# Optimization experiments

Hardware: AMD Instinct MI355X
Metric: run time of the kernel (lower is better)

The kernel has to match this reference:

```python
import jax, jax.numpy as jnp
import numpy as np

EPS = 1e-7

def squash(s, axis=-1):
    # s * ||s||^2 / (1 + ||s||^2) / ||s||
    sq_norm = jnp.sum(jnp.square(s), axis=axis, keepdims=True)
    scale = sq_norm / (1.0 + sq_norm) / jnp.sqrt(sq_norm + EPS)
    return scale * s

def setup_inputs() -> dict:
    key = jax.random.key(0)
    k1, k2 = jax.random.split(key)
    B, I, K = 64, 2048, 16   # batch, input_num_capsule, input_dim_capsule
    N, D = 32, 32            # num_capsule, dim_capsule
    inputs = jax.random.normal(k1, (B, I, K), dtype=jnp.float32)
    W = jax.random.normal(k2, (N, I, D, K), dtype=jnp.float32) * 0.05
    return {"inputs": inputs, "W": W}

def reference(inputs, W, routings=3):
    # u_hat[b,n,i,d] = sum_k inputs[b,i,k] * W[n,i,d,k]
    # (tile over n + per-sample batch_dot in the original, fused here)
    u_hat = jnp.einsum('bik,nidk->bnid', inputs, W)  # [B,N,I,D]
    B, N, I, D = u_hat.shape
    b = jnp.zeros((B, N, I), dtype=u_hat.dtype)
    outputs = None
    for r in range(routings):
        c = jax.nn.softmax(b, axis=1)                          # softmax over num_capsule
        s = jnp.einsum('bni,bnid->bnd', c, u_hat)              # weighted sum over input caps
        outputs = squash(s)                                    # [B,N,D]
        if r < routings - 1:
            b = b + jnp.einsum('bnd,bnid->bni', outputs, u_hat)  # agreement update
    return outputs
```

## Files before the change

kernel.cpp:

```cpp
#include <hip/hip_runtime.h>
#include <hip/hip_bf16.h>
#include <math.h>

#define B_ 64
#define I_ 2048
#define K_ 16
#define N_ 32
#define D_ 32
#define CH_ 32
#define SCH_ 16

typedef __attribute__((ext_vector_type(8))) short short8_t;
typedef __attribute__((ext_vector_type(4))) float f32x4_t;

#define OFF_INT   0u
#define OFF_CT    2097152u
#define OFF_BT    6291456u
#define OFF_SPART 10485760u
#define OFF_OUTT  11534336u
#define OFF_XFRAG 11599872u
#define OFF_WFS   12648448u
#define OFF_WFU   29425664u

__device__ __forceinline__ unsigned int pk_bf16(float lo, float hi) {
    union { __hip_bfloat162 h2; unsigned int u; } cv;
    cv.h2 = __float22bfloat162_rn(float2{lo, hi});
    return cv.u;
}

__global__ __launch_bounds__(256) void k_transpose(const float* __restrict__ in,
                                                   float* __restrict__ inT) {
    __shared__ float lds[B_][K_ + 1];
    const int i = blockIdx.x;
    const int t = threadIdx.x;
    const int b = t >> 2, kq = t & 3;
    const float4 v = *(const float4*)(in + ((size_t)b * I_ + i) * K_ + kq * 4);
    lds[b][kq * 4 + 0] = v.x; lds[b][kq * 4 + 1] = v.y;
    lds[b][kq * 4 + 2] = v.z; lds[b][kq * 4 + 3] = v.w;
    __syncthreads();
#pragma unroll
    for (int q = 0; q < 4; ++q) {
        const int j = t + q * 256;
        const int k = j >> 6, bb = j & 63;
        inT[(size_t)i * (K_ * B_) + j] = lds[bb][k];
    }
}

__global__ __launch_bounds__(256) void k_xfrag(const float* __restrict__ in,
                                               uint4* __restrict__ xfrag) {
    const int tid = blockIdx.x * 256 + threadIdx.x;
    const int l = tid & 63, kk = (tid >> 6) & 1023, m = tid >> 16;
    const int b = m * 16 + (l & 15), g = l >> 4;
    const int i = 2 * kk + (g >> 1), k0 = 8 * (g & 1);
    const float* src = in + ((size_t)b * I_ + i) * K_ + k0;
    const float4 f0 = *(const float4*)src;
    const float4 f1 = *(const float4*)(src + 4);
    uint4 o;
    o.x = pk_bf16(f0.x, f0.y); o.y = pk_bf16(f0.z, f0.w);
    o.z = pk_bf16(f1.x, f1.y); o.w = pk_bf16(f1.z, f1.w);
    xfrag[tid] = o;
}

__global__ __launch_bounds__(256) void k_wpack(const float* __restrict__ W,
                                               uint4* __restrict__ wfs,
                                               uint4* __restrict__ wfu) {
    __shared__ __align__(16) float lds[2048];
    const int c = blockIdx.x;
    const int n = blockIdx.y;
    const int t = threadIdx.x;
    const float4* s4 = (const float4*)(W + ((size_t)n * I_ + c * 4) * 512);
    float4* d4 = (float4*)lds;
    d4[t] = s4[t];
    d4[t + 256] = s4[t + 256];
    __syncthreads();
    {
        const int il = t >> 6, l = t & 63, g = l >> 4, kl = l & 15;
        const float* base = lds + il * 512;
        union { unsigned int u[4]; uint4 q; } o;
#pragma unroll
        for (int p = 0; p < 4; ++p)
            o.u[p] = pk_bf16(base[(8 * g + 2 * p) * 16 + kl],
                             base[(8 * g + 2 * p + 1) * 16 + kl]);
        wfu[((size_t)n * I_ + c * 4 + il) * 64 + l] = o.q;
    }
    {
        const int kkl = t >> 7, r = t & 127, nt = r >> 6, l = r & 63, g = l >> 4;
        const float* p = lds + kkl * 1024 + (g >> 1) * 512 + nt * 256
                         + (l & 15) * 16 + (g & 1) * 8;
        const float4 f0 = *(const float4*)p;
        const float4 f1 = *(const float4*)(p + 4);
        union { unsigned int u[4]; uint4 q; } o;
        o.u[0] = pk_bf16(f0.x, f0.y); o.u[1] = pk_bf16(f0.z, f0.w);
        o.u[2] = pk_bf16(f1.x, f1.y); o.u[3] = pk_bf16(f1.z, f1.w);
        wfs[(((size_t)n * 1024 + c * 2 + kkl) * 2 + nt) * 64 + l] = o.q;
    }
}

template<int UNIFORM>
__global__ __launch_bounds__(512, 2) void k_sweep_mfma(const uint4* __restrict__ wfs,
                                                       const uint4* __restrict__ xfrag,
                                                       const float* __restrict__ cT,
                                                       float* __restrict__ spart) {
    __shared__ float red[2][B_][D_ + 1];
    const int n = blockIdx.y, ch = blockIdx.x;
    const int t = threadIdx.x, w = t >> 6, l = t & 63;
    const int m = w >> 1, ks = w & 1;

    f32x4_t acc0 = {0.f, 0.f, 0.f, 0.f};
    f32x4_t acc1 = {0.f, 0.f, 0.f, 0.f};

    const uint4* xf = xfrag + (size_t)m * 65536 + l;
    const uint4* wf = wfs + (size_t)n * (1024 * 128) + l;
    const int kk0 = ch * 64 + ks * 32;

    for (int tt = 0; tt < 32; ++tt) {
        const int kk = kk0 + tt;
        union { uint4 q; unsigned int u[4]; } xv;
        xv.q = xf[(size_t)kk * 64];
        union { unsigned int u[4]; short8_t v; } af;
        if (UNIFORM) {
            af.u[0] = xv.u[0]; af.u[1] = xv.u[1];
            af.u[2] = xv.u[2]; af.u[3] = xv.u[3];
        } else {
            const float c = cT[((size_t)n * I_ + 2 * kk + (l >> 5)) * B_
                               + m * 16 + (l & 15)];
#pragma unroll
            for (int p = 0; p < 4; ++p) {
                const unsigned int uu = xv.u[p];
                const float lo = __uint_as_float(uu << 16);
                const float hi = __uint_as_float(uu & 0xffff0000u);
                af.u[p] = pk_bf16(lo * c, hi * c);
            }
        }
        union { uint4 q; short8_t v; } b0, b1;
        b0.q = wf[(size_t)kk * 128];
        b1.q = wf[(size_t)kk * 128 + 64];

        acc0 = __builtin_amdgcn_mfma_f32_16x16x32_bf16(af.v, b0.v, acc0, 0, 0, 0);
        acc1 = __builtin_amdgcn_mfma_f32_16x16x32_bf16(af.v, b1.v, acc1, 0, 0, 0);
    }

#pragma unroll
    for (int r = 0; r < 4; ++r) {
        const int row = m * 16 + (l >> 4) * 4 + r;
        red[ks][row][(l & 15)]      = acc0[r];
        red[ks][row][16 + (l & 15)] = acc1[r];
    }
    __syncthreads();
#pragma unroll
    for (int q = 0; q < 4; ++q) {
        const int j = q * 512 + t;
        const int b = j >> 5, d = j & 31;
        spart[((size_t)n * SCH_ + ch) * (B_ * D_) + j] = red[0][b][d] + red[1][b][d];
    }
}

template<int FINAL>
__global__ __launch_bounds__(256) void k_reduce(const float* __restrict__ spart,
                                                float* __restrict__ outT,
                                                float* __restrict__ out,
                                                float prescale) {
    const int gt = blockIdx.x * 256 + threadIdx.x;
    const int n = gt >> 11;
    const int rem = gt & 2047;
    const int b = rem >> 5, d = rem & 31;
    const float* sp = spart + (size_t)n * (SCH_ * B_ * D_) + rem;
    float s = 0.f;
#pragma unroll
    for (int p = 0; p < SCH_; ++p) s += sp[p * (B_ * D_)];
    s *= prescale;

    float sq = s * s;
#pragma unroll
    for (int off = 16; off >= 1; off >>= 1) sq += __shfl_xor(sq, off, 64);
    const float scale = sq / ((1.0f + sq) * sqrtf(sq + 1e-7f));
    const float o = scale * s;
    if (FINAL) {
        out[((size_t)b * N_ + n) * D_ + d] = o;
    } else {
        outT[((size_t)n * D_ + d) * B_ + b] = o;
    }
}

template<int FIRST>
__global__ __launch_bounds__(512, 2) void k_update_mfma(const uint4* __restrict__ wfu,
                                                        const float* __restrict__ inT,
                                                        const float* __restrict__ outT,
                                                        float* __restrict__ bT) {
    const int n = blockIdx.y, ch = blockIdx.x;
    const int t = threadIdx.x, w = t >> 6, l = t & 63;
    const int btile = w & 3;
    const int ig = w >> 2;
    const int g = l >> 4;
    const int kl = l & 15;

    union { unsigned int u[4]; short8_t v; } of;
    {
        const float* op = outT + (size_t)n * (D_ * B_) + btile * 16 + kl;
#pragma unroll
        for (int p = 0; p < 4; ++p) {
            const float e0 = op[(8 * g + 2 * p) * B_];
            const float e1 = op[(8 * g + 2 * p + 1) * B_];
            of.u[p] = pk_bf16(e0, e1);
        }
    }

    const uint4* wf = wfu + ((size_t)n * I_ + ch * 64 + ig * 32) * 64 + l;

    for (int tt = 0; tt < 32; ++tt) {
        const int i = ch * 64 + ig * 32 + tt;
        union { uint4 q; short8_t v; } af;
        af.q = wf[(size_t)tt * 64];
        f32x4_t acc = {0.f, 0.f, 0.f, 0.f};
        acc = __builtin_amdgcn_mfma_f32_16x16x32_bf16(af.v, of.v, acc, 0, 0, 0);
        float gp = 0.f;
        const float* xp = inT + (size_t)i * (K_ * B_) + btile * 16 + kl;
#pragma unroll
        for (int r = 0; r < 4; ++r)
            gp = fmaf(acc[r], xp[(4 * g + r) * B_], gp);
        gp += __shfl_xor(gp, 16, 64);
        gp += __shfl_xor(gp, 32, 64);
        if (l < 16) {
            const size_t bi = ((size_t)n * I_ + i) * B_ + btile * 16 + l;
            bT[bi] = FIRST ? gp : (bT[bi] + gp);
        }
    }
}

__global__ __launch_bounds__(256) void k_softmax(const float* __restrict__ bT,
                                                 float* __restrict__ cT) {
    const int t = threadIdx.x, w = t >> 6, lane = t & 63;
    const int i = blockIdx.x * 4 + w;
    float v[N_];
#pragma unroll
    for (int n = 0; n < N_; ++n) v[n] = bT[((size_t)n * I_ + i) * B_ + lane];
    float m = v[0];
#pragma unroll
    for (int n = 1; n < N_; ++n) m = fmaxf(m, v[n]);
    float sum = 0.f;
#pragma unroll
    for (int n = 0; n < N_; ++n) { v[n] = __expf(v[n] - m); sum += v[n]; }
    const float inv = 1.0f / sum;
#pragma unroll
    for (int n = 0; n < N_; ++n)
        cT[((size_t)n * I_ + i) * B_ + lane] = v[n] * inv;
}

extern "C" void kernel_launch(void* const* d_in, const int* in_sizes, int n_in,
                              void* d_out, int out_size, void* d_ws, size_t ws_size,
                              hipStream_t stream) {
    const float* inputs = (const float*)d_in[0];
    const float* W      = (const float*)d_in[1];
    float* out = (float*)d_out;
    float* ws  = (float*)d_ws;
    float* inT   = ws + OFF_INT;
    float* cT    = ws + OFF_CT;
    float* bT    = ws + OFF_BT;
    float* spart = ws + OFF_SPART;
    float* outT  = ws + OFF_OUTT;
    uint4* xfrag = (uint4*)(ws + OFF_XFRAG);
    uint4* wfs   = (uint4*)(ws + OFF_WFS);
    uint4* wfu   = (uint4*)(ws + OFF_WFU);

    k_transpose<<<I_, 256, 0, stream>>>(inputs, inT);
    k_xfrag<<<1024, 256, 0, stream>>>(inputs, xfrag);
    k_wpack<<<dim3(512, N_), 256, 0, stream>>>(W, wfs, wfu);
    k_sweep_mfma<1><<<dim3(SCH_, N_), 512, 0, stream>>>(wfs, xfrag, cT, spart);
    k_reduce<0><<<256, 256, 0, stream>>>(spart, outT, out, 1.0f / N_);
    k_update_mfma<1><<<dim3(CH_, N_), 512, 0, stream>>>(wfu, inT, outT, bT);
    k_softmax<<<I_ / 4, 256, 0, stream>>>(bT, cT);
    k_sweep_mfma<0><<<dim3(SCH_, N_), 512, 0, stream>>>(wfs, xfrag, cT, spart);
    k_reduce<0><<<256, 256, 0, stream>>>(spart, outT, out, 1.0f);
    k_update_mfma<0><<<dim3(CH_, N_), 512, 0, stream>>>(wfu, inT, outT, bT);
    k_softmax<<<I_ / 4, 256, 0, stream>>>(bT, cT);
    k_sweep_mfma<0><<<dim3(SCH_, N_), 512, 0, stream>>>(wfs, xfrag, cT, spart);
    k_reduce<1><<<256, 256, 0, stream>>>(spart, outT, out, 1.0f);
}
```

Baseline: 204.6 us.

## Fuse agreement update with softmax and merge input prep kernels

The agreement-update MFMA kernel is restructured so that each block handles two input capsules across all 32 output capsules. It then computes the softmax over n in registers and writes cT directly, which removes the separate softmax kernel and its bT re-read. The reduce kernel now writes the squashed outputs straight into a prepacked bf16 MFMA fragment layout, so the update kernel no longer gathers and converts outT. The transpose and xfrag kernels are merged into one prep pass that reads the inputs once. Together these cut three kernel launches and some global traffic, at the cost of a different grid shape and more register pressure from holding 32 values per lane.

```diff
diff --git a/kernel.cpp b/kernel.cpp
--- a/kernel.cpp
+++ b/kernel.cpp
@@ -7,7 +7,6 @@
 #define K_ 16
 #define N_ 32
 #define D_ 32
-#define CH_ 32
 #define SCH_ 16
 
 typedef __attribute__((ext_vector_type(8))) short short8_t;
@@ -17,7 +16,7 @@
 #define OFF_CT    2097152u
 #define OFF_BT    6291456u
 #define OFF_SPART 10485760u
-#define OFF_OUTT  11534336u
+#define OFF_OFRAG 11534336u
 #define OFF_XFRAG 11599872u
 #define OFF_WFS   12648448u
 #define OFF_WFU   29425664u
@@ -28,8 +27,9 @@
     return cv.u;
 }
 
-__global__ __launch_bounds__(256) void k_transpose(const float* __restrict__ in,
-                                                   float* __restrict__ inT) {
+__global__ __launch_bounds__(256) void k_prep(const float* __restrict__ in,
+                                              float* __restrict__ inT,
+                                              uint4* __restrict__ xfrag) {
     __shared__ float lds[B_][K_ + 1];
     const int i = blockIdx.x;
     const int t = threadIdx.x;
@@ -44,21 +44,15 @@
         const int k = j >> 6, bb = j & 63;
         inT[(size_t)i * (K_ * B_) + j] = lds[bb][k];
     }
-}
-
-__global__ __launch_bounds__(256) void k_xfrag(const float* __restrict__ in,
-                                               uint4* __restrict__ xfrag) {
-    const int tid = blockIdx.x * 256 + threadIdx.x;
-    const int l = tid & 63, kk = (tid >> 6) & 1023, m = tid >> 16;
-    const int b = m * 16 + (l & 15), g = l >> 4;
-    const int i = 2 * kk + (g >> 1), k0 = 8 * (g & 1);
-    const float* src = in + ((size_t)b * I_ + i) * K_ + k0;
-    const float4 f0 = *(const float4*)src;
-    const float4 f1 = *(const float4*)(src + 4);
-    uint4 o;
-    o.x = pk_bf16(f0.x, f0.y); o.y = pk_bf16(f0.z, f0.w);
-    o.z = pk_bf16(f1.x, f1.y); o.w = pk_bf16(f1.z, f1.w);
-    xfrag[tid] = o;
+    if (t < 128) {
+        const int m = t >> 5, r = t & 31, gl = r >> 4, kl = r & 15;
+        const int bb = m * 16 + kl, k0 = 8 * gl;
+        union { unsigned int u[4]; uint4 q; } o;
+#pragma unroll
+        for (int p = 0; p < 4; ++p)
+            o.u[p] = pk_bf16(lds[bb][k0 + 2 * p], lds[bb][k0 + 2 * p + 1]);
+        xfrag[((size_t)m * 1024 + (i >> 1)) * 64 + (2 * (i & 1) + gl) * 16 + kl] = o.q;
+    }
 }
 
 __global__ __launch_bounds__(256) void k_wpack(const float* __restrict__ W,
@@ -157,7 +151,7 @@
 
 template<int FINAL>
 __global__ __launch_bounds__(256) void k_reduce(const float* __restrict__ spart,
-                                                float* __restrict__ outT,
+                                                unsigned int* __restrict__ ofrag_u32,
                                                 float* __restrict__ out,
                                                 float prescale) {
     const int gt = blockIdx.x * 256 + threadIdx.x;
@@ -178,72 +172,68 @@
     if (FINAL) {
         out[((size_t)b * N_ + n) * D_ + d] = o;
     } else {
-        outT[((size_t)n * D_ + d) * B_ + b] = o;
+        const float o_next = __shfl_down(o, 1, 64);
+        if ((d & 1) == 0) {
+            const unsigned int val = pk_bf16(o, o_next);
+            const int l = (d >> 3) * 16 + (b & 15);
+            ofrag_u32[(((n * 4 + (b >> 4)) * 64) + l) * 4 + ((d & 7) >> 1)] = val;
+        }
     }
 }
 
 template<int FIRST>
-__global__ __launch_bounds__(512, 2) void k_update_mfma(const uint4* __restrict__ wfu,
-                                                        const float* __restrict__ inT,
-                                                        const float* __restrict__ outT,
-                                                        float* __restrict__ bT) {
-    const int n = blockIdx.y, ch = blockIdx.x;
+__global__ __launch_bounds__(512, 2) void k_updsm(const uint4* __restrict__ wfu,
+                                                  const float* __restrict__ inT,
+                                                  const uint4* __restrict__ ofrag,
+                                                  float* __restrict__ bT,
+                                                  float* __restrict__ cT) {
     const int t = threadIdx.x, w = t >> 6, l = t & 63;
     const int btile = w & 3;
-    const int ig = w >> 2;
-    const int g = l >> 4;
-    const int kl = l & 15;
-
-    union { unsigned int u[4]; short8_t v; } of;
+    const int i = blockIdx.x * 2 + (w >> 2);
+    const int g = l >> 4, kl = l & 15;
+    const int bp = btile * 16 + kl;
+
+    float x4[4];
     {
-        const float* op = outT + (size_t)n * (D_ * B_) + btile * 16 + kl;
-#pragma unroll
-        for (int p = 0; p < 4; ++p) {
-            const float e0 = op[(8 * g + 2 * p) * B_];
-            const float e1 = op[(8 * g + 2 * p + 1) * B_];
-            of.u[p] = pk_bf16(e0, e1);
-        }
-    }
-
-    const uint4* wf = wfu + ((size_t)n * I_ + ch * 64 + ig * 32) * 64 + l;
-
-    for (int tt = 0; tt < 32; ++tt) {
-        const int i = ch * 64 + ig * 32 + tt;
-        union { uint4 q; short8_t v; } af;
-        af.q = wf[(size_t)tt * 64];
+        const float* xp = inT + (size_t)i * (K_ * B_) + bp;
+#pragma unroll
+        for (int r = 0; r < 4; ++r) x4[r] = xp[(4 * g + r) * B_];
+    }
+
+    float bn[N_];
+#pragma unroll
+    for (int n = 0; n < N_; ++n) {
+        union { uint4 q; short8_t v; } of, af;
+        of.q = ofrag[(n * 4 + btile) * 64 + l];
+        af.q = wfu[((size_t)n * I_ + i) * 64 + l];
         f32x4_t acc = {0.f, 0.f, 0.f, 0.f};
         acc = __builtin_amdgcn_mfma_f32_16x16x32_bf16(af.v, of.v, acc, 0, 0, 0);
         float gp = 0.f;
-        const float* xp = inT + (size_t)i * (K_ * B_) + btile * 16 + kl;
-#pragma unroll
-        for (int r = 0; r < 4; ++r)
-            gp = fmaf(acc[r], xp[(4 * g + r) * B_], gp);
+#pragma unroll
+        for (int r = 0; r < 4; ++r) gp = fmaf(acc[r], x4[r], gp);
         gp += __shfl_xor(gp, 16, 64);
         gp += __shfl_xor(gp, 32, 64);
-        if (l < 16) {
-            const size_t bi = ((size_t)n * I_ + i) * B_ + btile * 16 + l;
-            bT[bi] = FIRST ? gp : (bT[bi] + gp);
+        const size_t bi = ((size_t)n * I_ + i) * B_ + bp;
+        if (FIRST) {
+            if (l < 16) bT[bi] = gp;
+        } else {
+            gp += bT[bi];
         }
-    }
-}
-
-__global__ __launch_bounds__(256) void k_softmax(const float* __restrict__ bT,
-                                                 float* __restrict__ cT) {
-    const int t = threadIdx.x, w = t >> 6, lane = t & 63;
-    const int i = blockIdx.x * 4 + w;
-    float v[N_];
-#pragma unroll
-    for (int n = 0; n < N_; ++n) v[n] = bT[((size_t)n * I_ + i) * B_ + lane];
-    float m = v[0];
-#pragma unroll
-    for (int n = 1; n < N_; ++n) m = fmaxf(m, v[n]);
+        bn[n] = gp;
+    }
+
+    float mx = bn[0];
+#pragma unroll
+    for (int n = 1; n < N_; ++n) mx = fmaxf(mx, bn[n]);
     float sum = 0.f;
 #pragma unroll
-    for (int n = 0; n < N_; ++n) { v[n] = __expf(v[n] - m); sum += v[n]; }
+    for (int n = 0; n < N_; ++n) { bn[n] = __expf(bn[n] - mx); sum += bn[n]; }
     const float inv = 1.0f / sum;
-#pragma unroll
-    for (int n = 0; n < N_; ++n)
-        cT[((size_t)n * I_ + i) * B_ + lane] = v[n] * inv;
+    if (l < 16) {
+#pragma unroll
+        for (int n = 0; n < N_; ++n)
+            cT[((size_t)n * I_ + i) * B_ + bp] = bn[n] * inv;
+    }
 }
 
 extern "C" void kernel_launch(void* const* d_in, const int* in_sizes, int n_in,
@@ -257,22 +247,20 @@
     float* cT    = ws + OFF_CT;
     float* bT    = ws + OFF_BT;
     float* spart = ws + OFF_SPART;
-    float* outT  = ws + OFF_OUTT;
+    unsigned int* ofrag_u32 = (unsigned int*)(ws + OFF_OFRAG);
+    uint4* ofrag = (uint4*)(ws + OFF_OFRAG);
     uint4* xfrag = (uint4*)(ws + OFF_XFRAG);
     uint4* wfs   = (uint4*)(ws + OFF_WFS);
     uint4* wfu   = (uint4*)(ws + OFF_WFU);
 
-    k_transpose<<<I_, 256, 0, stream>>>(inputs, inT);
-    k_xfrag<<<1024, 256, 0, stream>>>(inputs, xfrag);
+    k_prep<<<I_, 256, 0, stream>>>(inputs, inT, xfrag);
     k_wpack<<<dim3(512, N_), 256, 0, stream>>>(W, wfs, wfu);
     k_sweep_mfma<1><<<dim3(SCH_, N_), 512, 0, stream>>>(wfs, xfrag, cT, spart);
-    k_reduce<0><<<256, 256, 0, stream>>>(spart, outT, out, 1.0f / N_);
-    k_update_mfma<1><<<dim3(CH_, N_), 512, 0, stream>>>(wfu, inT, outT, bT);
-    k_softmax<<<I_ / 4, 256, 0, stream>>>(bT, cT);
+    k_reduce<0><<<256, 256, 0, stream>>>(spart, ofrag_u32, out, 1.0f / N_);
+    k_updsm<1><<<I_ / 2, 512, 0, stream>>>(wfu, inT, ofrag, bT, cT);
     k_sweep_mfma<0><<<dim3(SCH_, N_), 512, 0, stream>>>(wfs, xfrag, cT, spart);
-    k_reduce<0><<<256, 256, 0, stream>>>(spart, outT, out, 1.0f);
-    k_update_mfma<0><<<dim3(CH_, N_), 512, 0, stream>>>(wfu, inT, outT, bT);
-    k_softmax<<<I_ / 4, 256, 0, stream>>>(bT, cT);
+    k_reduce<0><<<256, 256, 0, stream>>>(spart, ofrag_u32, out, 1.0f);
+    k_updsm<0><<<I_ / 2, 512, 0, stream>>>(wfu, inT, ofrag, bT, cT);
     k_sweep_mfma<0><<<dim3(SCH_, N_), 512, 0, stream>>>(wfs, xfrag, cT, spart);
-    k_reduce<1><<<256, 256, 0, stream>>>(spart, outT, out, 1.0f);
-}
+    k_reduce<1><<<256, 256, 0, stream>>>(spart, ofrag_u32, out, 1.0f);
+}
```

Measured after the change: 175.6 us. 14.2% less time.
